# Kernel tuning notes

Measured on AMD Instinct MI355X. Metric: run time of the kernel, lower is better.

Reference implementation:

```python
import jax, jax.numpy as jnp
import numpy as np

T = 2.0          # hardcoded in __init__ (self.T = 2)
EPSILON = 0.1    # sinkhorn_loss default
N_ITERS = 10     # sinkhorn_loss default passed to sinkhorn_normalized
COST_CLIP = 10.0
TINY = 1e-8

B, S, V = 16, 512, 4096


def setup_inputs() -> dict:
    key = jax.random.key(0)
    k1, k2 = jax.random.split(key)
    y_s = jax.random.normal(k1, (B, S, V), dtype=jnp.float32)
    y_t = jax.random.normal(k2, (B, S, V), dtype=jnp.float32)
    return {"y_s": y_s, "y_t": y_t}


def _cdist_l1(x, y):
    # x, y: [S, V] -> [S, S]; row-streamed via lax.map to avoid a [S,S,V] intermediate
    return jax.lax.map(lambda xi: jnp.sum(jnp.abs(xi[None, :] - y), axis=-1), x)


def _sinkhorn_loss(x, y):
    # x, y: [S, V] softmax probabilities for one sample
    Wxy = _cdist_l1(x, y)                                  # [S, S]
    K = jnp.exp(-jnp.minimum(Wxy, COST_CLIP) / EPSILON)
    P = jnp.nan_to_num(K, nan=TINY, posinf=1e6, neginf=-1e6) + TINY
    for _ in range(N_ITERS):
        P = P / jnp.maximum(jnp.sum(P, axis=1, keepdims=True), TINY)
        P = jnp.nan_to_num(P, nan=TINY)
        P = P / jnp.maximum(jnp.sum(P, axis=0, keepdims=True), TINY)
        P = jnp.nan_to_num(P, nan=TINY)
    return jnp.sum(P * Wxy)


def reference(y_s, y_t):
    p_s = jax.nn.softmax(y_s / T, axis=-1)
    p_t = jax.nn.softmax(y_t / T, axis=-1)
    p_s = jnp.nan_to_num(p_s, nan=TINY)
    p_t = jnp.nan_to_num(p_t, nan=TINY)
    per_sample = jax.vmap(_sinkhorn_loss)(p_s, p_t)        # [B]
    # forward accumulates 0.001 * loss_i and divides by the number of valid samples
    return jnp.mean(0.001 * per_sample)
```

## Files before the change

### kernel.cpp

```cpp
#include <hip/hip_runtime.h>

#define B_ 16
#define S_ 512
#define V_ 4096

typedef unsigned int uint;
typedef unsigned short ushort;
typedef unsigned char u8;


__device__ __forceinline__ uint sad8(uint a, uint b, uint c) {
#if __has_builtin(__builtin_amdgcn_sad_u8)
    return __builtin_amdgcn_sad_u8(a, b, c);
#else
    uint s = c;
#pragma unroll
    for (int i = 0; i < 4; ++i) {
        uint x = (a >> (8 * i)) & 0xFFu, y = (b >> (8 * i)) & 0xFFu;
        s += x > y ? x - y : y - x;
    }
    return s;
#endif
}

__device__ __forceinline__ float bflo(uint p) { return __uint_as_float(p << 16); }
__device__ __forceinline__ float bfhi(uint p) { return __uint_as_float(p & 0xFFFF0000u); }

__device__ __forceinline__ ushort f2bf(float f) {
    uint u = __float_as_uint(f);
    u = (u + 0x7FFFu + ((u >> 16) & 1u)) >> 16;
    return (ushort)u;
}

__device__ __forceinline__ float waveMax(float v) {
#pragma unroll
    for (int o = 32; o; o >>= 1) v = fmaxf(v, __shfl_xor(v, o, 64));
    return v;
}
__device__ __forceinline__ float waveSum(float v) {
#pragma unroll
    for (int o = 32; o; o >>= 1) v += __shfl_xor(v, o, 64);
    return v;
}

#define GLOAD_LDS16(g, l)                                                      \
    __builtin_amdgcn_global_load_lds(                                          \
        (const __attribute__((address_space(1))) uint*)(g),                    \
        (__attribute__((address_space(3))) uint*)(l), 16, 0, 0)

#define QSCALE 65536.0f
#define QINV   1.52587890625e-5f

__global__ __launch_bounds__(256) void softmax_kernel(
        const float* __restrict__ ys, const float* __restrict__ yt,
        u8* __restrict__ qs, u8* __restrict__ qt) {
    const int row = blockIdx.x;
    const float* in = blockIdx.y ? yt : ys;
    u8* out = blockIdx.y ? qt : qs;
    const float* px = in + (size_t)row * V_;
    u8* po = out + (size_t)row * V_;
    const int tid = threadIdx.x;

    float4 v4[4];
    float m = -3.4e38f;
#pragma unroll
    for (int i = 0; i < 4; ++i) {
        v4[i] = ((const float4*)px)[tid + 256 * i];
        m = fmaxf(m, fmaxf(fmaxf(v4[i].x, v4[i].y), fmaxf(v4[i].z, v4[i].w)));
    }
    __shared__ float redm[4], reds[4];
    float wm = waveMax(m);
    if ((tid & 63) == 0) redm[tid >> 6] = wm;
    __syncthreads();
    const float rm = fmaxf(fmaxf(redm[0], redm[1]), fmaxf(redm[2], redm[3]));

    float e[16];
    float s = 0.f;
#pragma unroll
    for (int i = 0; i < 4; ++i) {
        const float* f = (const float*)&v4[i];
#pragma unroll
        for (int k = 0; k < 4; ++k) {
            float ev = __expf((f[k] - rm) * 0.5f);
            e[i * 4 + k] = ev;
            s += ev;
        }
    }
    float wsm = waveSum(s);
    if ((tid & 63) == 0) reds[tid >> 6] = wsm;
    __syncthreads();
    const float inv = 1.0f / (reds[0] + reds[1] + reds[2] + reds[3]);

#pragma unroll
    for (int i = 0; i < 4; ++i) {
        uint pk = 0;
#pragma unroll
        for (int k = 0; k < 4; ++k) {
            float p = e[i * 4 + k] * inv;
            uint q = (uint)fminf(p * QSCALE + 0.5f, 255.f);
            pk |= q << (8 * k);
        }
        ((uint*)po)[tid + 256 * i] = pk;
    }
}

#define TI 128
#define TJ 128
#define KCB 128

__global__ __launch_bounds__(256) void pairwise_kernel(
        const u8* __restrict__ qs, const u8* __restrict__ qt,
        ushort* __restrict__ Wb, ushort* __restrict__ Kb) {
    const int b = blockIdx.z;
    const int tR = blockIdx.y * TI;
    const int tC = blockIdx.x * TJ;
    const u8* xrow = qs + (size_t)b * S_ * V_ + (size_t)tR * V_;
    const u8* yrow = qt + (size_t)b * S_ * V_ + (size_t)tC * V_;
    const int tid = threadIdx.x;
    const int lane = tid & 63, wv = tid >> 6;
    const int tx = tid & 15, ty = tid >> 4;

    __shared__ u8 xs[2][TI * KCB];
    __shared__ u8 ysm[2][TJ * KCB];

    const int rs = lane >> 3;
    const int coff = ((lane & 7) ^ rs) << 4;
    const int s0 = wv * 4;
    const size_t g0 = (size_t)((s0 + 0) * 8 + rs) * V_ + coff;
    const size_t g1 = (size_t)((s0 + 1) * 8 + rs) * V_ + coff;
    const size_t g2 = (size_t)((s0 + 2) * 8 + rs) * V_ + coff;
    const size_t g3 = (size_t)((s0 + 3) * 8 + rs) * V_ + coff;

#define STAGE_V6(bufidx, koff)                                                 \
    {                                                                          \
        GLOAD_LDS16(xrow + (koff) + g0, &xs[bufidx][(s0 + 0) * 1024]);         \
        GLOAD_LDS16(xrow + (koff) + g1, &xs[bufidx][(s0 + 1) * 1024]);         \
        GLOAD_LDS16(xrow + (koff) + g2, &xs[bufidx][(s0 + 2) * 1024]);         \
        GLOAD_LDS16(xrow + (koff) + g3, &xs[bufidx][(s0 + 3) * 1024]);         \
        GLOAD_LDS16(yrow + (koff) + g0, &ysm[bufidx][(s0 + 0) * 1024]);        \
        GLOAD_LDS16(yrow + (koff) + g1, &ysm[bufidx][(s0 + 1) * 1024]);        \
        GLOAD_LDS16(yrow + (koff) + g2, &ysm[bufidx][(s0 + 2) * 1024]);        \
        GLOAD_LDS16(yrow + (koff) + g3, &ysm[bufidx][(s0 + 3) * 1024]);        \
    }

    uint acc[8][8];
#pragma unroll
    for (int r = 0; r < 8; ++r)
#pragma unroll
        for (int c = 0; c < 8; ++c) acc[r][c] = 0u;

    const int aswz = ty & 7;
    const int bswz = tx & 7;

    STAGE_V6(0, 0);
    __syncthreads();

    for (int c0 = 0; c0 < V_ / KCB; ++c0) {
        const int cur = c0 & 1;
        if (c0 + 1 < V_ / KCB)
            STAGE_V6(cur ^ 1, (size_t)(c0 + 1) * KCB);
#pragma unroll
        for (int kk = 0; kk < 8; ++kk) {
            const int ao = (kk ^ aswz) << 4;
            const int bo = (kk ^ bswz) << 4;
            uint4 Af[8], Bf[8];
#pragma unroll
            for (int r = 0; r < 8; ++r)
                Af[r] = *(const uint4*)&xs[cur][(ty + 16 * r) * KCB + ao];
#pragma unroll
            for (int c = 0; c < 8; ++c)
                Bf[c] = *(const uint4*)&ysm[cur][(tx + 16 * c) * KCB + bo];
#pragma unroll
            for (int r = 0; r < 8; ++r)
#pragma unroll
                for (int c = 0; c < 8; ++c) {
                    uint t = sad8(Af[r].x, Bf[c].x, acc[r][c]);
                    t = sad8(Af[r].y, Bf[c].y, t);
                    t = sad8(Af[r].z, Bf[c].z, t);
                    acc[r][c] = sad8(Af[r].w, Bf[c].w, t);
                }
        }
        __syncthreads();
    }

#pragma unroll
    for (int r = 0; r < 8; ++r) {
        const int i = tR + ty + 16 * r;
        const size_t base = ((size_t)b * S_ + i) * S_;
#pragma unroll
        for (int c = 0; c < 8; ++c) {
            const int j = tC + tx + 16 * c;
            const float w = fminf((float)acc[r][c] * QINV, 10.f);
            Wb[base + j] = f2bf(w);
            Kb[base + j] = f2bf(__expf(-10.f * w) + 1e-8f);
        }
    }
#undef STAGE_V6
}

__global__ __launch_bounds__(1024) void sink_block(
        const ushort* __restrict__ Kb, const ushort* __restrict__ Wb,
        float* __restrict__ out) {
    const int b = blockIdx.x;
    const int tid = threadIdx.x, lane = tid & 63, wv = tid >> 6;
    const int ch = lane & 31, rq = lane >> 5;

    __shared__ float vp[S_];
    __shared__ float uls[S_];
    __shared__ float cwp[16][S_];
    __shared__ float redw[16];

    if (tid < S_) { vp[tid] = 1.f; uls[tid] = 1.f; }
    __syncthreads();

    const ushort* Kl = Kb + (size_t)b * S_ * S_;
    const int chB = ch * 16;

    for (int it = 0; it < 10; ++it) {
        const float4 v0 = *(const float4*)&vp[chB];
        const float4 v1 = *(const float4*)&vp[chB + 4];
        const float4 v2 = *(const float4*)&vp[chB + 8];
        const float4 v3 = *(const float4*)&vp[chB + 12];
        float4 c0 = make_float4(0.f, 0.f, 0.f, 0.f);
        float4 c1 = c0, c2 = c0, c3 = c0;

#pragma unroll 2
        for (int g = 0; g < 16; ++g) {
            const int i = wv * 32 + g * 2 + rq;
            const ushort* kp = Kl + (size_t)i * S_ + chB;
            const uint4 ka = *(const uint4*)kp;
            const uint4 kc = *(const uint4*)(kp + 8);
            float d0 = 0.f, d1 = 0.f;
            d0 = fmaf(bflo(ka.x), v0.x, d0); d0 = fmaf(bfhi(ka.x), v0.y, d0);
            d0 = fmaf(bflo(ka.y), v0.z, d0); d0 = fmaf(bfhi(ka.y), v0.w, d0);
            d0 = fmaf(bflo(ka.z), v1.x, d0); d0 = fmaf(bfhi(ka.z), v1.y, d0);
            d0 = fmaf(bflo(ka.w), v1.z, d0); d0 = fmaf(bfhi(ka.w), v1.w, d0);
            d1 = fmaf(bflo(kc.x), v2.x, d1); d1 = fmaf(bfhi(kc.x), v2.y, d1);
            d1 = fmaf(bflo(kc.y), v2.z, d1); d1 = fmaf(bfhi(kc.y), v2.w, d1);
            d1 = fmaf(bflo(kc.z), v3.x, d1); d1 = fmaf(bfhi(kc.z), v3.y, d1);
            d1 = fmaf(bflo(kc.w), v3.z, d1); d1 = fmaf(bfhi(kc.w), v3.w, d1);
            float dot = d0 + d1;
            dot += __shfl_xor(dot, 1, 64);
            dot += __shfl_xor(dot, 2, 64);
            dot += __shfl_xor(dot, 4, 64);
            dot += __shfl_xor(dot, 8, 64);
            dot += __shfl_xor(dot, 16, 64);
            const float up = uls[i];
            const float un = up / fmaxf(up * dot, 1e-8f);
            if (ch == 0) uls[i] = un;
            c0.x = fmaf(un, bflo(ka.x), c0.x); c0.y = fmaf(un, bfhi(ka.x), c0.y);
            c0.z = fmaf(un, bflo(ka.y), c0.z); c0.w = fmaf(un, bfhi(ka.y), c0.w);
            c1.x = fmaf(un, bflo(ka.z), c1.x); c1.y = fmaf(un, bfhi(ka.z), c1.y);
            c1.z = fmaf(un, bflo(ka.w), c1.z); c1.w = fmaf(un, bfhi(ka.w), c1.w);
            c2.x = fmaf(un, bflo(kc.x), c2.x); c2.y = fmaf(un, bfhi(kc.x), c2.y);
            c2.z = fmaf(un, bflo(kc.y), c2.z); c2.w = fmaf(un, bfhi(kc.y), c2.w);
            c3.x = fmaf(un, bflo(kc.z), c3.x); c3.y = fmaf(un, bfhi(kc.z), c3.y);
            c3.z = fmaf(un, bflo(kc.w), c3.z); c3.w = fmaf(un, bfhi(kc.w), c3.w);
        }
        c0.x += __shfl_xor(c0.x, 32, 64); c0.y += __shfl_xor(c0.y, 32, 64);
        c0.z += __shfl_xor(c0.z, 32, 64); c0.w += __shfl_xor(c0.w, 32, 64);
        c1.x += __shfl_xor(c1.x, 32, 64); c1.y += __shfl_xor(c1.y, 32, 64);
        c1.z += __shfl_xor(c1.z, 32, 64); c1.w += __shfl_xor(c1.w, 32, 64);
        c2.x += __shfl_xor(c2.x, 32, 64); c2.y += __shfl_xor(c2.y, 32, 64);
        c2.z += __shfl_xor(c2.z, 32, 64); c2.w += __shfl_xor(c2.w, 32, 64);
        c3.x += __shfl_xor(c3.x, 32, 64); c3.y += __shfl_xor(c3.y, 32, 64);
        c3.z += __shfl_xor(c3.z, 32, 64); c3.w += __shfl_xor(c3.w, 32, 64);
        if (rq == 0) {
            *(float4*)&cwp[wv][chB] = c0;
            *(float4*)&cwp[wv][chB + 4] = c1;
        } else {
            *(float4*)&cwp[wv][chB + 8] = c2;
            *(float4*)&cwp[wv][chB + 12] = c3;
        }
        __syncthreads();
        if (tid < S_) {
            float s = 0.f;
#pragma unroll
            for (int t = 0; t < 16; ++t) s += cwp[t][tid];
            const float vv = vp[tid];
            vp[tid] = vv / fmaxf(vv * s, 1e-8f);
        }
        __syncthreads();
    }

    const float4 v0 = *(const float4*)&vp[chB];
    const float4 v1 = *(const float4*)&vp[chB + 4];
    const float4 v2 = *(const float4*)&vp[chB + 8];
    const float4 v3 = *(const float4*)&vp[chB + 12];
    const ushort* Wl = Wb + (size_t)b * S_ * S_;
    float accl = 0.f;
#pragma unroll 2
    for (int g = 0; g < 16; ++g) {
        const int i = wv * 32 + g * 2 + rq;
        const ushort* kp = Kl + (size_t)i * S_ + chB;
        const ushort* wp = Wl + (size_t)i * S_ + chB;
        const uint4 ka = *(const uint4*)kp;
        const uint4 kc = *(const uint4*)(kp + 8);
        const uint4 wa = *(const uint4*)wp;
        const uint4 wc = *(const uint4*)(wp + 8);
        float r0 = 0.f, r1 = 0.f;
        r0 = fmaf(bflo(ka.x) * v0.x, bflo(wa.x), r0);
        r0 = fmaf(bfhi(ka.x) * v0.y, bfhi(wa.x), r0);
        r0 = fmaf(bflo(ka.y) * v0.z, bflo(wa.y), r0);
        r0 = fmaf(bfhi(ka.y) * v0.w, bfhi(wa.y), r0);
        r0 = fmaf(bflo(ka.z) * v1.x, bflo(wa.z), r0);
        r0 = fmaf(bfhi(ka.z) * v1.y, bfhi(wa.z), r0);
        r0 = fmaf(bflo(ka.w) * v1.z, bflo(wa.w), r0);
        r0 = fmaf(bfhi(ka.w) * v1.w, bfhi(wa.w), r0);
        r1 = fmaf(bflo(kc.x) * v2.x, bflo(wc.x), r1);
        r1 = fmaf(bfhi(kc.x) * v2.y, bfhi(wc.x), r1);
        r1 = fmaf(bflo(kc.y) * v2.z, bflo(wc.y), r1);
        r1 = fmaf(bfhi(kc.y) * v2.w, bfhi(wc.y), r1);
        r1 = fmaf(bflo(kc.z) * v3.x, bflo(wc.z), r1);
        r1 = fmaf(bfhi(kc.z) * v3.y, bfhi(wc.z), r1);
        r1 = fmaf(bflo(kc.w) * v3.z, bflo(wc.w), r1);
        r1 = fmaf(bfhi(kc.w) * v3.w, bfhi(wc.w), r1);
        float rp = r0 + r1;
        rp += __shfl_xor(rp, 1, 64);
        rp += __shfl_xor(rp, 2, 64);
        rp += __shfl_xor(rp, 4, 64);
        rp += __shfl_xor(rp, 8, 64);
        rp += __shfl_xor(rp, 16, 64);
        if (ch == 0) accl = fmaf(uls[i], rp, accl);
    }
    accl += __shfl_xor(accl, 32, 64);
    if (lane == 0) redw[wv] = accl;
    __syncthreads();
    if (tid == 0) {
        float s = 0.f;
#pragma unroll
        for (int t = 0; t < 16; ++t) s += redw[t];
        atomicAdd(out, s * (0.001f / 16.f));
    }
}

extern "C" void kernel_launch(void* const* d_in, const int* in_sizes, int n_in,
                              void* d_out, int out_size, void* d_ws, size_t ws_size,
                              hipStream_t stream) {
    const float* ys = (const float*)d_in[0];
    const float* yt = (const float*)d_in[1];
    float* out = (float*)d_out;

    char* w = (char*)d_ws;
    u8* qs = (u8*)w;
    u8* qt = qs + (size_t)B_ * S_ * V_;
    ushort* Wb = (ushort*)(qt + (size_t)B_ * S_ * V_);
    ushort* Kb = Wb + (size_t)B_ * S_ * S_;

    (void)hipMemsetAsync(out, 0, sizeof(float), stream);

    softmax_kernel<<<dim3(8192, 2), 256, 0, stream>>>(ys, yt, qs, qt);
    pairwise_kernel<<<dim3(4, 4, 16), 256, 0, stream>>>(qs, qt, Wb, Kb);
    sink_block<<<16, 1024, 0, stream>>>(Kb, Wb, out);
}
```

Before: 552.7 us.

## Use 512 threads per pairwise tile and pad Sinkhorn shared vectors

The pairwise L1 kernel now runs 512 threads per 128x128 tile. Each thread accumulates a 4x8 block instead of 8x8, and each wave stages half as many rows. This adds waves to hide LDS and SAD latency, since only 256 blocks cover the device, but it lowers per-thread reuse of loaded fragments. Separately, the Sinkhorn kernel pads its v and column-partial shared arrays to a stride of 20 floats per 16-column chunk, aiming to cut LDS bank conflicts on the float4 accesses.

Result: no change. 553.8 us (+0.2%).

```diff
diff --git a/kernel.cpp b/kernel.cpp
--- a/kernel.cpp
+++ b/kernel.cpp
@@ -108,7 +108,7 @@
 #define TJ 128
 #define KCB 128
 
-__global__ __launch_bounds__(256) void pairwise_kernel(
+__global__ __launch_bounds__(512) void pairwise_kernel(
         const u8* __restrict__ qs, const u8* __restrict__ qt,
         ushort* __restrict__ Wb, ushort* __restrict__ Kb) {
     const int b = blockIdx.z;
@@ -125,53 +125,47 @@
 
     const int rs = lane >> 3;
     const int coff = ((lane & 7) ^ rs) << 4;
-    const int s0 = wv * 4;
+    const int s0 = wv * 2;
     const size_t g0 = (size_t)((s0 + 0) * 8 + rs) * V_ + coff;
     const size_t g1 = (size_t)((s0 + 1) * 8 + rs) * V_ + coff;
-    const size_t g2 = (size_t)((s0 + 2) * 8 + rs) * V_ + coff;
-    const size_t g3 = (size_t)((s0 + 3) * 8 + rs) * V_ + coff;
-
-#define STAGE_V6(bufidx, koff)                                                 \
+
+#define STAGE_V7(bufidx, koff)                                                 \
     {                                                                          \
         GLOAD_LDS16(xrow + (koff) + g0, &xs[bufidx][(s0 + 0) * 1024]);         \
         GLOAD_LDS16(xrow + (koff) + g1, &xs[bufidx][(s0 + 1) * 1024]);         \
-        GLOAD_LDS16(xrow + (koff) + g2, &xs[bufidx][(s0 + 2) * 1024]);         \
-        GLOAD_LDS16(xrow + (koff) + g3, &xs[bufidx][(s0 + 3) * 1024]);         \
         GLOAD_LDS16(yrow + (koff) + g0, &ysm[bufidx][(s0 + 0) * 1024]);        \
         GLOAD_LDS16(yrow + (koff) + g1, &ysm[bufidx][(s0 + 1) * 1024]);        \
-        GLOAD_LDS16(yrow + (koff) + g2, &ysm[bufidx][(s0 + 2) * 1024]);        \
-        GLOAD_LDS16(yrow + (koff) + g3, &ysm[bufidx][(s0 + 3) * 1024]);        \
-    }
-
-    uint acc[8][8];
-#pragma unroll
-    for (int r = 0; r < 8; ++r)
+    }
+
+    uint acc[4][8];
+#pragma unroll
+    for (int r = 0; r < 4; ++r)
 #pragma unroll
         for (int c = 0; c < 8; ++c) acc[r][c] = 0u;
 
     const int aswz = ty & 7;
     const int bswz = tx & 7;
 
-    STAGE_V6(0, 0);
+    STAGE_V7(0, 0);
     __syncthreads();
 
     for (int c0 = 0; c0 < V_ / KCB; ++c0) {
         const int cur = c0 & 1;
         if (c0 + 1 < V_ / KCB)
-            STAGE_V6(cur ^ 1, (size_t)(c0 + 1) * KCB);
+            STAGE_V7(cur ^ 1, (size_t)(c0 + 1) * KCB);
 #pragma unroll
         for (int kk = 0; kk < 8; ++kk) {
             const int ao = (kk ^ aswz) << 4;
             const int bo = (kk ^ bswz) << 4;
-            uint4 Af[8], Bf[8];
-#pragma unroll
-            for (int r = 0; r < 8; ++r)
-                Af[r] = *(const uint4*)&xs[cur][(ty + 16 * r) * KCB + ao];
+            uint4 Af[4], Bf[8];
+#pragma unroll
+            for (int r = 0; r < 4; ++r)
+                Af[r] = *(const uint4*)&xs[cur][(ty + 32 * r) * KCB + ao];
 #pragma unroll
             for (int c = 0; c < 8; ++c)
                 Bf[c] = *(const uint4*)&ysm[cur][(tx + 16 * c) * KCB + bo];
 #pragma unroll
-            for (int r = 0; r < 8; ++r)
+            for (int r = 0; r < 4; ++r)
 #pragma unroll
                 for (int c = 0; c < 8; ++c) {
                     uint t = sad8(Af[r].x, Bf[c].x, acc[r][c]);
@@ -184,8 +178,8 @@
     }
 
 #pragma unroll
-    for (int r = 0; r < 8; ++r) {
-        const int i = tR + ty + 16 * r;
+    for (int r = 0; r < 4; ++r) {
+        const int i = tR + ty + 32 * r;
         const size_t base = ((size_t)b * S_ + i) * S_;
 #pragma unroll
         for (int c = 0; c < 8; ++c) {
@@ -195,8 +189,10 @@
             Kb[base + j] = f2bf(__expf(-10.f * w) + 1e-8f);
         }
     }
-#undef STAGE_V6
-}
+#undef STAGE_V7
+}
+
+#define VG 20
 
 __global__ __launch_bounds__(1024) void sink_block(
         const ushort* __restrict__ Kb, const ushort* __restrict__ Wb,
@@ -205,29 +201,31 @@
     const int tid = threadIdx.x, lane = tid & 63, wv = tid >> 6;
     const int ch = lane & 31, rq = lane >> 5;
 
-    __shared__ float vp[S_];
+    __shared__ float vp[32 * VG];
     __shared__ float uls[S_];
-    __shared__ float cwp[16][S_];
+    __shared__ float cwp[16][32 * VG];
     __shared__ float redw[16];
 
-    if (tid < S_) { vp[tid] = 1.f; uls[tid] = 1.f; }
+    for (int m = tid; m < 32 * VG; m += 1024) vp[m] = 1.f;
+    if (tid < S_) uls[tid] = 1.f;
     __syncthreads();
 
     const ushort* Kl = Kb + (size_t)b * S_ * S_;
-    const int chB = ch * 16;
+    const int col0 = ch * 16;
+    const int pB = ch * VG;
 
     for (int it = 0; it < 10; ++it) {
-        const float4 v0 = *(const float4*)&vp[chB];
-        const float4 v1 = *(const float4*)&vp[chB + 4];
-        const float4 v2 = *(const float4*)&vp[chB + 8];
-        const float4 v3 = *(const float4*)&vp[chB + 12];
+        const float4 v0 = *(const float4*)&vp[pB];
+        const float4 v1 = *(const float4*)&vp[pB + 4];
+        const float4 v2 = *(const float4*)&vp[pB + 8];
+        const float4 v3 = *(const float4*)&vp[pB + 12];
         float4 c0 = make_float4(0.f, 0.f, 0.f, 0.f);
         float4 c1 = c0, c2 = c0, c3 = c0;
 
 #pragma unroll 2
         for (int g = 0; g < 16; ++g) {
             const int i = wv * 32 + g * 2 + rq;
-            const ushort* kp = Kl + (size_t)i * S_ + chB;
+            const ushort* kp = Kl + (size_t)i * S_ + col0;
             const uint4 ka = *(const uint4*)kp;
             const uint4 kc = *(const uint4*)(kp + 8);
             float d0 = 0.f, d1 = 0.f;
@@ -266,34 +264,35 @@
         c3.x += __shfl_xor(c3.x, 32, 64); c3.y += __shfl_xor(c3.y, 32, 64);
         c3.z += __shfl_xor(c3.z, 32, 64); c3.w += __shfl_xor(c3.w, 32, 64);
         if (rq == 0) {
-            *(float4*)&cwp[wv][chB] = c0;
-            *(float4*)&cwp[wv][chB + 4] = c1;
+            *(float4*)&cwp[wv][pB] = c0;
+            *(float4*)&cwp[wv][pB + 4] = c1;
         } else {
-            *(float4*)&cwp[wv][chB + 8] = c2;
-            *(float4*)&cwp[wv][chB + 12] = c3;
+            *(float4*)&cwp[wv][pB + 8] = c2;
+            *(float4*)&cwp[wv][pB + 12] = c3;
         }
         __syncthreads();
         if (tid < S_) {
+            const int a = (tid >> 4) * VG + (tid & 15);
             float s = 0.f;
 #pragma unroll
-            for (int t = 0; t < 16; ++t) s += cwp[t][tid];
-            const float vv = vp[tid];
-            vp[tid] = vv / fmaxf(vv * s, 1e-8f);
+            for (int t = 0; t < 16; ++t) s += cwp[t][a];
+            const float vv = vp[a];
+            vp[a] = vv / fmaxf(vv * s, 1e-8f);
         }
         __syncthreads();
     }
 
-    const float4 v0 = *(const float4*)&vp[chB];
-    const float4 v1 = *(const float4*)&vp[chB + 4];
-    const float4 v2 = *(const float4*)&vp[chB + 8];
-    const float4 v3 = *(const float4*)&vp[chB + 12];
+    const float4 v0 = *(const float4*)&vp[pB];
+    const float4 v1 = *(const float4*)&vp[pB + 4];
+    const float4 v2 = *(const float4*)&vp[pB + 8];
+    const float4 v3 = *(const float4*)&vp[pB + 12];
     const ushort* Wl = Wb + (size_t)b * S_ * S_;
     float accl = 0.f;
 #pragma unroll 2
     for (int g = 0; g < 16; ++g) {
         const int i = wv * 32 + g * 2 + rq;
-        const ushort* kp = Kl + (size_t)i * S_ + chB;
-        const ushort* wp = Wl + (size_t)i * S_ + chB;
+        const ushort* kp = Kl + (size_t)i * S_ + col0;
+        const ushort* wp = Wl + (size_t)i * S_ + col0;
         const uint4 ka = *(const uint4*)kp;
         const uint4 kc = *(const uint4*)(kp + 8);
         const uint4 wa = *(const uint4*)wp;
@@ -350,6 +349,6 @@
     (void)hipMemsetAsync(out, 0, sizeof(float), stream);
 
     softmax_kernel<<<dim3(8192, 2), 256, 0, stream>>>(ys, yt, qs, qt);
-    pairwise_kernel<<<dim3(4, 4, 16), 256, 0, stream>>>(qs, qt, Wb, Kb);
+    pairwise_kernel<<<dim3(4, 4, 16), 512, 0, stream>>>(qs, qt, Wb, Kb);
     sink_block<<<16, 1024, 0, stream>>>(Kb, Wb, out);
 }
```
